# Performance work log

Measured on AMD Instinct MI355X. Metric: run time of the kernel, lower is better.

Reference implementation:

```python
import jax, jax.numpy as jnp
import numpy as np

N, C, V, T = 16, 32, 512, 64
H, EMB, D = 4, 64, 16
OUT_C = 64
BN_EPS = 1e-5


def setup_inputs() -> dict:
    key = jax.random.key(0)
    ks = jax.random.split(key, 12)
    x = jax.random.normal(ks[0], (N, C, V, T), dtype=jnp.float32)
    t_in = jax.random.uniform(ks[1], (N, T), dtype=jnp.float32)
    # random-walk-like supports; scaled so chained nconv hops stay O(1)
    A0 = jax.random.normal(ks[2], (V, V), dtype=jnp.float32) * (V ** -0.5)
    A1 = jax.random.normal(ks[3], (V, V), dtype=jnp.float32) * (V ** -0.5)
    A2 = jax.random.normal(ks[4], (V, V), dtype=jnp.float32) * (V ** -0.5)
    factors = jax.random.normal(ks[5], (H,), dtype=jnp.float32) * 0.1
    Wq = jax.random.normal(ks[6], (H, EMB, D), dtype=jnp.float32) * (EMB ** -0.5)
    Wk = jax.random.normal(ks[7], (H, EMB, D), dtype=jnp.float32) * (EMB ** -0.5)
    GC_IN = 7 * C  # (order*support_len + 1) * in_channels
    W_out = jax.random.normal(ks[8], (OUT_C, GC_IN), dtype=jnp.float32) * (GC_IN ** -0.5)
    b_out = jnp.zeros((OUT_C,), dtype=jnp.float32)
    W_res = jax.random.normal(ks[9], (OUT_C, C), dtype=jnp.float32) * (C ** -0.5)
    b_res = jnp.zeros((OUT_C,), dtype=jnp.float32)
    bn_gamma = jnp.ones((OUT_C,), dtype=jnp.float32)
    bn_beta = jnp.zeros((OUT_C,), dtype=jnp.float32)
    bn_mean = jnp.zeros((OUT_C,), dtype=jnp.float32)
    bn_var = jnp.ones((OUT_C,), dtype=jnp.float32)
    alpha = jnp.full((1,), 0.25, dtype=jnp.float32)  # PReLU init
    return dict(x=x, t_in=t_in, A0=A0, A1=A1, A2=A2, factors=factors,
                Wq=Wq, Wk=Wk, W_out=W_out, b_out=b_out,
                W_res=W_res, b_res=b_res, bn_gamma=bn_gamma, bn_beta=bn_beta,
                bn_mean=bn_mean, bn_var=bn_var, alpha=alpha)


def reference(x, t_in, A0, A1, A2, factors, Wq, Wk, W_out, b_out,
              W_res, b_res, bn_gamma, bn_beta, bn_mean, bn_var, alpha):
    # --- learnEmbedding, all heads at once: emb[b,h,t,f] ---
    div = jnp.arange(0, EMB, 2, dtype=x.dtype)           # [EMB/2]
    div_term = jnp.exp(div[None, :] * factors[:, None])  # [H, EMB/2]
    phase = jnp.einsum('bt,hf->bhtf', t_in, div_term)    # [N,H,T,EMB/2]
    emb = jnp.concatenate([jnp.sin(phase), jnp.cos(phase)], axis=-1)  # [N,H,T,EMB]
    # --- ATT per head (t_out=None => q_emb == k_emb) ---
    q = jnp.einsum('bhtf,hfd->bhtd', emb, Wq)
    k = jnp.einsum('bhtf,hfd->bhtd', emb, Wk)
    att = jax.nn.softmax(jnp.einsum('bhtd,bhpd->bhtp', q, k) / (D ** 0.5), axis=-1)  # [N,H,T,T]
    # --- temporal mixing, summed over heads (matches per-head += loop) ---
    xt = jnp.einsum('ncvt,nhpt->ncvp', x, att)           # [N,C,V,T]
    # --- gcn: diffusion over 3 supports, order 2 ---
    outs = [xt]
    for A in (A0, A1, A2):
        x1 = jnp.einsum('ncvl,vw->ncwl', xt, A)
        x2 = jnp.einsum('ncvl,vw->ncwl', x1, A)
        outs.extend([x1, x2])
    h = jnp.concatenate(outs, axis=1)                    # [N,7C,V,T]
    # --- 1x1 output projection ---
    y = jnp.einsum('ncvt,oc->novt', h, W_out) + b_out[None, :, None, None]
    # --- residual branch: 1x1 conv + BatchNorm (eval) ---
    r = jnp.einsum('ncvt,oc->novt', x, W_res) + b_res[None, :, None, None]
    r = (r - bn_mean[None, :, None, None]) * jax.lax.rsqrt(bn_var + BN_EPS)[None, :, None, None]
    r = r * bn_gamma[None, :, None, None] + bn_beta[None, :, None, None]
    # --- residual add + PReLU (dropout is identity in eval) ---
    out = y + r
    out = jnp.where(out > 0, out, alpha[0] * out)
    return out
```

## Files before the change

### kernel.cpp

```cpp
#include <hip/hip_runtime.h>

namespace {
constexpr int N_ = 16, C_ = 32, V_ = 512, T_ = 64;
constexpr int H_ = 4, D_ = 16, OC_ = 64;
constexpr int EMB_ = 64;
constexpr int GCIN_ = 7 * C_;
constexpr int TV_ = T_ * V_;
}

typedef _Float16 f16x8 __attribute__((ext_vector_type(8)));
typedef _Float16 f16x4 __attribute__((ext_vector_type(4)));
typedef float f32x4 __attribute__((ext_vector_type(4)));

__global__ __launch_bounds__(64) void att_kernel(
    const float* __restrict__ t_in, const float* __restrict__ factors,
    const float* __restrict__ Wq, const float* __restrict__ Wk,
    float* __restrict__ att)
{
    const int n = blockIdx.x >> 2;
    const int h = blockIdx.x & 3;
    const int t = threadIdx.x;

    __shared__ float wq_l[EMB_][D_];
    __shared__ float wk_l[EMB_][D_];
    __shared__ float k_l[T_][D_ + 1];

#pragma unroll
    for (int d = 0; d < D_; ++d) {
        wq_l[t][d] = Wq[(h * EMB_ + t) * D_ + d];
        wk_l[t][d] = Wk[(h * EMB_ + t) * D_ + d];
    }
    __syncthreads();

    const float tv = t_in[n * T_ + t];
    const float fh = factors[h];
    float emb[EMB_];
#pragma unroll
    for (int j = 0; j < 32; ++j) {
        float dt = __expf((float)(2 * j) * fh);
        float ph = tv * dt;
        float s, c;
        __sincosf(ph, &s, &c);
        emb[j] = s;
        emb[j + 32] = c;
    }

    float q[D_];
#pragma unroll
    for (int d = 0; d < D_; ++d) {
        float aq = 0.f, ak = 0.f;
#pragma unroll
        for (int f = 0; f < EMB_; ++f) {
            aq += emb[f] * wq_l[f][d];
            ak += emb[f] * wk_l[f][d];
        }
        q[d] = aq;
        k_l[t][d] = ak;
    }
    __syncthreads();

    float L[T_];
    float m = -1e30f;
#pragma unroll
    for (int j = 0; j < T_; ++j) {
        float a = 0.f;
#pragma unroll
        for (int d = 0; d < D_; ++d) a += q[d] * k_l[j][d];
        a *= 0.25f;
        L[j] = a;
        m = fmaxf(m, a);
    }
    float ssum = 0.f;
#pragma unroll
    for (int j = 0; j < T_; ++j) {
        float e = __expf(L[j] - m);
        L[j] = e;
        ssum += e;
    }
    const float inv = 1.f / ssum;
    float* arow = att + (((size_t)(n * H_ + h) * T_ + t) * T_);
#pragma unroll
    for (int j = 0; j < T_; ++j) arow[j] = L[j] * inv;
}

__global__ __launch_bounds__(256) void sred_kernel(
    const float* __restrict__ att, float* __restrict__ S)
{
    int g = blockIdx.x * 256 + threadIdx.x;
    if (g >= N_ * T_ * T_) return;
    int n = g / (T_ * T_);
    int ij = g - n * (T_ * T_);
    float a = 0.f;
#pragma unroll
    for (int h = 0; h < H_; ++h) a += att[(size_t)(n * H_ + h) * (T_ * T_) + ij];
    S[g] = a;
}

__global__ __launch_bounds__(256) void prepAt_kernel(
    const float* __restrict__ A0, const float* __restrict__ A1,
    const float* __restrict__ A2, _Float16* __restrict__ At16)
{
    const int s = blockIdx.z;
    const float* A = (s == 0) ? A0 : ((s == 1) ? A1 : A2);
    const int v0 = blockIdx.y * 32, w0 = blockIdx.x * 32;
    const int tid = threadIdx.x;
    __shared__ float sT[32][33];
#pragma unroll
    for (int k = 0; k < 4; ++k) {
        int lin = k * 256 + tid;
        int i = lin >> 5, w = lin & 31;
        sT[i][w] = A[(size_t)(v0 + i) * V_ + w0 + w];
    }
    __syncthreads();
#pragma unroll
    for (int k = 0; k < 4; ++k) {
        int lin = k * 256 + tid;
        int j = lin >> 5, i = lin & 31;
        At16[(size_t)s * V_ * V_ + (size_t)(w0 + j) * V_ + v0 + i] = (_Float16)sT[i][j];
    }
}

__global__ __launch_bounds__(256) void prepxT_kernel(
    const float* __restrict__ x, _Float16* __restrict__ xT, int n0)
{
    const int b = blockIdx.z;
    const int v0 = blockIdx.x * 32;
    const int t0 = blockIdx.y * 32;
    const int tid = threadIdx.x;
    __shared__ float sT[32][33];
    const float* xb = x + ((size_t)(n0 * C_) + b) * (size_t)(V_ * T_);
    {
        int vi = tid >> 3, tq = tid & 7;
        *(float4*)&sT[vi][tq * 4] = *(const float4*)&xb[(size_t)(v0 + vi) * T_ + t0 + tq * 4];
    }
    __syncthreads();
    {
        int tj = tid >> 3, vq = tid & 7;
        f16x4 o4;
        o4[0] = (_Float16)sT[vq * 4 + 0][tj];
        o4[1] = (_Float16)sT[vq * 4 + 1][tj];
        o4[2] = (_Float16)sT[vq * 4 + 2][tj];
        o4[3] = (_Float16)sT[vq * 4 + 3][tj];
        *(f16x4*)&xT[(size_t)b * TV_ + (size_t)(t0 + tj) * V_ + v0 + vq * 4] = o4;
    }
}

__global__ __launch_bounds__(256) void prepW_kernel(
    const float* __restrict__ W_out, const float* __restrict__ b_out,
    const float* __restrict__ W_res, const float* __restrict__ b_res,
    const float* __restrict__ gamma, const float* __restrict__ beta,
    const float* __restrict__ mean, const float* __restrict__ var,
    _Float16* __restrict__ Wcat, float* __restrict__ bias)
{
    const int tid = threadIdx.x;
    const int o = tid & 63;
    const int kb = tid >> 6;
    const float rs = gamma[o] * rsqrtf(var[o] + 1e-5f);
    for (int kk = 0; kk < 64; ++kk) {
        int k = kb * 64 + kk;
        float w = (k < GCIN_) ? W_out[o * GCIN_ + k] : rs * W_res[o * C_ + (k - GCIN_)];
        Wcat[o * 256 + k] = (_Float16)w;
    }
    if (tid < 64) bias[tid] = b_out[tid] + beta[tid] + rs * (b_res[tid] - mean[tid]);
}

__global__ __launch_bounds__(256) void xtT_kernel(
    const float* __restrict__ x, const float* __restrict__ S,
    _Float16* __restrict__ XT, int n0)
{
    const int b = blockIdx.y;
    const int n = n0 + b / C_;
    const int lane = threadIdx.x & 63;
    const int wav = threadIdx.x >> 6;
    const int vbase = blockIdx.x * 256 + wav * 64;
    const int row16 = lane & 15;
    const int kg = lane >> 4;

    const float* Sn = S + (size_t)n * (T_ * T_);
    const float* xb = x + ((size_t)(n0 * C_) + b) * (V_ * T_);

    f32x4 acc[4][4];
#pragma unroll
    for (int i = 0; i < 4; ++i)
#pragma unroll
        for (int j = 0; j < 4; ++j) acc[i][j] = (f32x4){0.f, 0.f, 0.f, 0.f};

#pragma unroll
    for (int ks = 0; ks < 2; ++ks) {
        f16x8 a[4], bf[4];
#pragma unroll
        for (int mt = 0; mt < 4; ++mt) {
            const float* p = xb + (size_t)(vbase + mt * 16 + row16) * T_ + ks * 32 + kg * 8;
            float4 u = *(const float4*)p;
            float4 w = *(const float4*)(p + 4);
            f16x8 t8;
            t8[0] = (_Float16)u.x; t8[1] = (_Float16)u.y; t8[2] = (_Float16)u.z; t8[3] = (_Float16)u.w;
            t8[4] = (_Float16)w.x; t8[5] = (_Float16)w.y; t8[6] = (_Float16)w.z; t8[7] = (_Float16)w.w;
            a[mt] = t8;
        }
#pragma unroll
        for (int nt = 0; nt < 4; ++nt) {
            const float* p = Sn + (size_t)(nt * 16 + row16) * T_ + ks * 32 + kg * 8;
            float4 u = *(const float4*)p;
            float4 w = *(const float4*)(p + 4);
            f16x8 t8;
            t8[0] = (_Float16)u.x; t8[1] = (_Float16)u.y; t8[2] = (_Float16)u.z; t8[3] = (_Float16)u.w;
            t8[4] = (_Float16)w.x; t8[5] = (_Float16)w.y; t8[6] = (_Float16)w.z; t8[7] = (_Float16)w.w;
            bf[nt] = t8;
        }
#pragma unroll
        for (int nt = 0; nt < 4; ++nt)
#pragma unroll
            for (int mt = 0; mt < 4; ++mt)
                acc[mt][nt] = __builtin_amdgcn_mfma_f32_16x16x32_f16(a[mt], bf[nt], acc[mt][nt], 0, 0, 0);
    }

    _Float16* Yb = XT + (size_t)b * TV_;
#pragma unroll
    for (int mt = 0; mt < 4; ++mt)
#pragma unroll
        for (int nt = 0; nt < 4; ++nt) {
            int p = nt * 16 + row16;
            int v = vbase + mt * 16 + kg * 4;
            f16x4 h;
            h[0] = (_Float16)acc[mt][nt][0];
            h[1] = (_Float16)acc[mt][nt][1];
            h[2] = (_Float16)acc[mt][nt][2];
            h[3] = (_Float16)acc[mt][nt][3];
            *(f16x4*)&Yb[(size_t)p * V_ + v] = h;
        }
}

__global__ __launch_bounds__(512) void hopf_kernel(
    const _Float16* __restrict__ At16, _Float16* __restrict__ Hb,
    unsigned long long ASZ)
{
    const int bp = blockIdx.x;
    const int s = blockIdx.y;
    const int tid = threadIdx.x;
    const int lane = tid & 63;
    const int wav = tid >> 6;
    const int wbase = wav * 64;
    const int row16 = lane & 15;
    const int kg = lane >> 4;

    __shared__ _Float16 xs0[T_ * V_];
    __shared__ _Float16 xs1[T_ * V_];

    const _Float16* At = At16 + (size_t)s * V_ * V_;
    const int b0 = bp * 2;
    const _Float16* Xb0 = Hb + (size_t)b0 * TV_;
    const _Float16* Xb1 = Hb + (size_t)(b0 + 1) * TV_;
    _Float16* Y1a = Hb + (size_t)(1 + 2 * s) * ASZ + (size_t)b0 * TV_;
    _Float16* Y1b = Y1a + TV_;
    _Float16* Y2a = Hb + (size_t)(2 + 2 * s) * ASZ + (size_t)b0 * TV_;
    _Float16* Y2b = Y2a + TV_;

    const _Float16* ax = At + (size_t)(wbase + row16) * V_ + kg * 8;

    f32x4 acc0[4][4], acc1[4][4];
    f16x8 aC[4], aN[4];

#pragma unroll
    for (int k = 0; k < 8; ++k) {
        int lin = k * 512 + tid;
        int t = lin >> 6;
        int v8 = (lin & 63) << 3;
        int byte = (t * V_ + v8) * 2;
        f16x8 v0v = *(const f16x8*)&Xb0[(size_t)t * V_ + v8];
        f16x8 v1v = *(const f16x8*)&Xb1[(size_t)t * V_ + v8];
        *(f16x8*)((char*)xs0 + (byte ^ ((t & 7) << 4))) = v0v;
        *(f16x8*)((char*)xs1 + (byte ^ ((t & 7) << 4))) = v1v;
    }
    __syncthreads();

#pragma unroll
    for (int i = 0; i < 4; ++i)
#pragma unroll
        for (int j = 0; j < 4; ++j) {
            acc0[i][j] = (f32x4){0.f, 0.f, 0.f, 0.f};
            acc1[i][j] = (f32x4){0.f, 0.f, 0.f, 0.f};
        }
#pragma unroll
    for (int i = 0; i < 4; ++i)
        aC[i] = *(const f16x8*)(ax + (size_t)i * 16 * V_);

#pragma unroll
    for (int it = 0; it < 16; ++it) {
        const int v0 = it * 32;
        if (it < 15) {
#pragma unroll
            for (int i = 0; i < 4; ++i)
                aN[i] = *(const f16x8*)(ax + (size_t)i * 16 * V_ + v0 + 32);
        }
        f16x8 b0v[4], b1v[4];
#pragma unroll
        for (int nt = 0; nt < 4; ++nt) {
            int t = nt * 16 + row16;
            int byte = (t * V_ + v0 + kg * 8) * 2;
            b0v[nt] = *(const f16x8*)((const char*)xs0 + (byte ^ ((t & 7) << 4)));
            b1v[nt] = *(const f16x8*)((const char*)xs1 + (byte ^ ((t & 7) << 4)));
        }
        __builtin_amdgcn_s_setprio(1);
#pragma unroll
        for (int nt = 0; nt < 4; ++nt)
#pragma unroll
            for (int mt = 0; mt < 4; ++mt) {
                acc0[mt][nt] = __builtin_amdgcn_mfma_f32_16x16x32_f16(aC[mt], b0v[nt], acc0[mt][nt], 0, 0, 0);
                acc1[mt][nt] = __builtin_amdgcn_mfma_f32_16x16x32_f16(aC[mt], b1v[nt], acc1[mt][nt], 0, 0, 0);
            }
        __builtin_amdgcn_s_setprio(0);
#pragma unroll
        for (int i = 0; i < 4; ++i) aC[i] = aN[i];
    }
    __syncthreads();

#pragma unroll
    for (int mt = 0; mt < 4; ++mt)
#pragma unroll
        for (int nt = 0; nt < 4; ++nt) {
            int t = nt * 16 + row16;
            int w = wbase + mt * 16 + kg * 4;
            int byte = (t * V_ + w) * 2;
            f16x4 h0, h1;
            h0[0] = (_Float16)acc0[mt][nt][0]; h0[1] = (_Float16)acc0[mt][nt][1];
            h0[2] = (_Float16)acc0[mt][nt][2]; h0[3] = (_Float16)acc0[mt][nt][3];
            h1[0] = (_Float16)acc1[mt][nt][0]; h1[1] = (_Float16)acc1[mt][nt][1];
            h1[2] = (_Float16)acc1[mt][nt][2]; h1[3] = (_Float16)acc1[mt][nt][3];
            *(f16x4*)((char*)xs0 + (byte ^ ((t & 7) << 4))) = h0;
            *(f16x4*)((char*)xs1 + (byte ^ ((t & 7) << 4))) = h1;
        }
    __syncthreads();

#pragma unroll
    for (int mt = 0; mt < 4; ++mt)
#pragma unroll
        for (int nt = 0; nt < 4; ++nt) {
            int t = nt * 16 + row16;
            int w = wbase + mt * 16 + kg * 4;
            f16x4 h0;
            h0[0] = (_Float16)acc0[mt][nt][0]; h0[1] = (_Float16)acc0[mt][nt][1];
            h0[2] = (_Float16)acc0[mt][nt][2]; h0[3] = (_Float16)acc0[mt][nt][3];
            *(f16x4*)&Y1a[(size_t)t * V_ + w] = h0;
        }
#pragma unroll
    for (int mt = 0; mt < 4; ++mt)
#pragma unroll
        for (int nt = 0; nt < 4; ++nt) {
            int t = nt * 16 + row16;
            int w = wbase + mt * 16 + kg * 4;
            f16x4 h1;
            h1[0] = (_Float16)acc1[mt][nt][0]; h1[1] = (_Float16)acc1[mt][nt][1];
            h1[2] = (_Float16)acc1[mt][nt][2]; h1[3] = (_Float16)acc1[mt][nt][3];
            *(f16x4*)&Y1b[(size_t)t * V_ + w] = h1;
        }

#pragma unroll
    for (int i = 0; i < 4; ++i)
#pragma unroll
        for (int j = 0; j < 4; ++j) {
            acc0[i][j] = (f32x4){0.f, 0.f, 0.f, 0.f};
            acc1[i][j] = (f32x4){0.f, 0.f, 0.f, 0.f};
        }
#pragma unroll
    for (int i = 0; i < 4; ++i)
        aC[i] = *(const f16x8*)(ax + (size_t)i * 16 * V_);

#pragma unroll
    for (int it = 0; it < 16; ++it) {
        const int v0 = it * 32;
        if (it < 15) {
#pragma unroll
            for (int i = 0; i < 4; ++i)
                aN[i] = *(const f16x8*)(ax + (size_t)i * 16 * V_ + v0 + 32);
        }
        f16x8 b0v[4], b1v[4];
#pragma unroll
        for (int nt = 0; nt < 4; ++nt) {
            int t = nt * 16 + row16;
            int byte = (t * V_ + v0 + kg * 8) * 2;
            b0v[nt] = *(const f16x8*)((const char*)xs0 + (byte ^ ((t & 7) << 4)));
            b1v[nt] = *(const f16x8*)((const char*)xs1 + (byte ^ ((t & 7) << 4)));
        }
        __builtin_amdgcn_s_setprio(1);
#pragma unroll
        for (int nt = 0; nt < 4; ++nt)
#pragma unroll
            for (int mt = 0; mt < 4; ++mt) {
                acc0[mt][nt] = __builtin_amdgcn_mfma_f32_16x16x32_f16(aC[mt], b0v[nt], acc0[mt][nt], 0, 0, 0);
                acc1[mt][nt] = __builtin_amdgcn_mfma_f32_16x16x32_f16(aC[mt], b1v[nt], acc1[mt][nt], 0, 0, 0);
            }
        __builtin_amdgcn_s_setprio(0);
#pragma unroll
        for (int i = 0; i < 4; ++i) aC[i] = aN[i];
    }

#pragma unroll
    for (int mt = 0; mt < 4; ++mt)
#pragma unroll
        for (int nt = 0; nt < 4; ++nt) {
            int t = nt * 16 + row16;
            int w = wbase + mt * 16 + kg * 4;
            f16x4 h0;
            h0[0] = (_Float16)acc0[mt][nt][0]; h0[1] = (_Float16)acc0[mt][nt][1];
            h0[2] = (_Float16)acc0[mt][nt][2]; h0[3] = (_Float16)acc0[mt][nt][3];
            *(f16x4*)&Y2a[(size_t)t * V_ + w] = h0;
        }
#pragma unroll
    for (int mt = 0; mt < 4; ++mt)
#pragma unroll
        for (int nt = 0; nt < 4; ++nt) {
            int t = nt * 16 + row16;
            int w = wbase + mt * 16 + kg * 4;
            f16x4 h1;
            h1[0] = (_Float16)acc1[mt][nt][0]; h1[1] = (_Float16)acc1[mt][nt][1];
            h1[2] = (_Float16)acc1[mt][nt][2]; h1[3] = (_Float16)acc1[mt][nt][3];
            *(f16x4*)&Y2b[(size_t)t * V_ + w] = h1;
        }
}

__global__ __launch_bounds__(256) void epi_kernel(
    const _Float16* __restrict__ H, unsigned long long ASZ,
    const _Float16* __restrict__ Wcat, const float* __restrict__ bias,
    const float* __restrict__ alpha_p, float* __restrict__ out, int n0)
{
    const int v0 = blockIdx.x * 32;
    const int t0 = blockIdx.y * 8;
    const int nl = blockIdx.z;
    const int ng = n0 + nl;
    const int tid = threadIdx.x;
    const int lane = tid & 63;
    const int wv = tid >> 6;
    const int row16 = lane & 15;
    const int kg = lane >> 4;

    f32x4 acc[2][2][4];
#pragma unroll
    for (int j = 0; j < 2; ++j)
#pragma unroll
        for (int vs = 0; vs < 2; ++vs)
#pragma unroll
            for (int mt = 0; mt < 4; ++mt) acc[j][vs][mt] = (f32x4){0.f, 0.f, 0.f, 0.f};

    const size_t pb = ((size_t)(nl * C_ + kg * 8)) * TV_
                    + (size_t)(t0 + wv * 2) * V_ + v0 + row16;

#pragma unroll
    for (int ks = 0; ks < 8; ++ks) {
        const _Float16* Hk = H + (size_t)ks * ASZ;
        f16x8 a[4];
#pragma unroll
        for (int mt = 0; mt < 4; ++mt)
            a[mt] = *(const f16x8*)(Wcat + (mt * 16 + row16) * 256 + ks * 32 + kg * 8);
#pragma unroll
        for (int j = 0; j < 2; ++j)
#pragma unroll
            for (int vs = 0; vs < 2; ++vs) {
                const _Float16* hp = Hk + pb + (size_t)j * V_ + vs * 16;
                f16x8 bf;
#pragma unroll
                for (int e = 0; e < 8; ++e) bf[e] = hp[(size_t)e * TV_];
#pragma unroll
                for (int mt = 0; mt < 4; ++mt)
                    acc[j][vs][mt] = __builtin_amdgcn_mfma_f32_16x16x32_f16(a[mt], bf, acc[j][vs][mt], 0, 0, 0);
            }
    }

    __shared__ float sC[16 * 33 * 9];
    const float al = alpha_p[0];
    const int ot = tid >> 4;
    const int vvt = tid & 15;

    for (int mt = 0; mt < 4; ++mt) {
#pragma unroll
        for (int j = 0; j < 2; ++j)
#pragma unroll
            for (int vs = 0; vs < 2; ++vs)
#pragma unroll
                for (int r = 0; r < 4; ++r)
                    sC[((kg * 4 + r) * 33 + vs * 16 + row16) * 9 + wv * 2 + j] = acc[j][vs][mt][r];
        __syncthreads();
        const float bo = bias[mt * 16 + ot];
#pragma unroll
        for (int vh = 0; vh < 2; ++vh) {
            const int vl = vvt + vh * 16;
            float vals[8];
#pragma unroll
            for (int tt = 0; tt < 8; ++tt) {
                float u = sC[(ot * 33 + vl) * 9 + tt] + bo;
                vals[tt] = u > 0.f ? u : al * u;
            }
            float* op = out + (((size_t)ng * OC_ + mt * 16 + ot) * V_ + v0 + vl) * T_ + t0;
            *(float4*)&op[0] = make_float4(vals[0], vals[1], vals[2], vals[3]);
            *(float4*)&op[4] = make_float4(vals[4], vals[5], vals[6], vals[7]);
        }
        __syncthreads();
    }
}

extern "C" void kernel_launch(void* const* d_in, const int* in_sizes, int n_in,
                              void* d_out, int out_size, void* d_ws, size_t ws_size,
                              hipStream_t stream)
{
    const float* x       = (const float*)d_in[0];
    const float* t_in    = (const float*)d_in[1];
    const float* A0      = (const float*)d_in[2];
    const float* A1      = (const float*)d_in[3];
    const float* A2      = (const float*)d_in[4];
    const float* factors = (const float*)d_in[5];
    const float* Wq      = (const float*)d_in[6];
    const float* Wk      = (const float*)d_in[7];
    const float* W_out   = (const float*)d_in[8];
    const float* b_out   = (const float*)d_in[9];
    const float* W_res   = (const float*)d_in[10];
    const float* b_res   = (const float*)d_in[11];
    const float* gamma   = (const float*)d_in[12];
    const float* beta    = (const float*)d_in[13];
    const float* mean    = (const float*)d_in[14];
    const float* var     = (const float*)d_in[15];
    const float* alpha   = (const float*)d_in[16];
    float* out = (float*)d_out;

    float* att = (float*)d_ws;
    float* S    = att + (size_t)N_ * H_ * T_ * T_;
    float* bias = S + (size_t)N_ * T_ * T_;
    _Float16* At16 = (_Float16*)(bias + 64);
    _Float16* Wcat = At16 + (size_t)3 * V_ * V_;
    _Float16* Hbase = Wcat + (size_t)64 * 256;

    const size_t fixed = ((size_t)N_ * H_ * T_ * T_ + (size_t)N_ * T_ * T_ + 64) * 4
                       + ((size_t)3 * V_ * V_ + 64 * 256) * 2;
    int Nc = 16;
    while (Nc > 1 && fixed + (size_t)8 * Nc * C_ * T_ * V_ * 2 > ws_size) Nc >>= 1;
    const size_t ASZ = (size_t)Nc * C_ * T_ * V_;

    att_kernel<<<N_ * H_, 64, 0, stream>>>(t_in, factors, Wq, Wk, att);
    sred_kernel<<<(N_ * T_ * T_ + 255) / 256, 256, 0, stream>>>(att, S);
    prepAt_kernel<<<dim3(16, 16, 3), 256, 0, stream>>>(A0, A1, A2, At16);
    prepW_kernel<<<1, 256, 0, stream>>>(W_out, b_out, W_res, b_res,
                                        gamma, beta, mean, var, Wcat, bias);

    for (int n0 = 0; n0 < N_; n0 += Nc) {
        const int nsl = Nc * C_;
        xtT_kernel<<<dim3(2, nsl), 256, 0, stream>>>(x, S, Hbase, n0);
        prepxT_kernel<<<dim3(16, 2, nsl), 256, 0, stream>>>(x, Hbase + (size_t)7 * ASZ, n0);
        hopf_kernel<<<dim3(nsl / 2, 3), 512, 0, stream>>>(At16, Hbase, (unsigned long long)ASZ);
        epi_kernel<<<dim3(16, 8, Nc), 256, 0, stream>>>(
            Hbase, (unsigned long long)ASZ, Wcat, bias, alpha, out, n0);
    }
}
```

Measured before the change: 495.1 us.

## Interleave channel pairs in fp16 intermediate buffers for wider epilogue loads

Changes the fp16 intermediate layout so each pair of channels is interleaved element-wise. The producers (xtT, prepxT, hopf) now process two channels per block and write 16-byte vectors, hopf de-interleaves into LDS, and the epilogue reads channel pairs as 2-element loads instead of 8 scalar strided loads. This is meant to cut scattered narrow global loads in the epilogue and halve the store instruction count. It also removes the s_setprio hints around the MFMA blocks in hopf and adds shuffle work when filling LDS.

```diff
diff --git a/kernel.cpp b/kernel.cpp
--- a/kernel.cpp
+++ b/kernel.cpp
@@ -10,6 +10,7 @@
 
 typedef _Float16 f16x8 __attribute__((ext_vector_type(8)));
 typedef _Float16 f16x4 __attribute__((ext_vector_type(4)));
+typedef _Float16 f16x2 __attribute__((ext_vector_type(2)));
 typedef float f32x4 __attribute__((ext_vector_type(4)));
 
 __global__ __launch_bounds__(64) void att_kernel(
@@ -123,25 +124,29 @@
 __global__ __launch_bounds__(256) void prepxT_kernel(
     const float* __restrict__ x, _Float16* __restrict__ xT, int n0)
 {
-    const int b = blockIdx.z;
+    const int q = blockIdx.z;
     const int v0 = blockIdx.x * 32;
     const int t0 = blockIdx.y * 32;
     const int tid = threadIdx.x;
-    __shared__ float sT[32][33];
-    const float* xb = x + ((size_t)(n0 * C_) + b) * (size_t)(V_ * T_);
+    __shared__ float sT0[32][33];
+    __shared__ float sT1[32][33];
+    const float* xb0 = x + ((size_t)(n0 * C_) + 2 * q) * (size_t)(V_ * T_);
+    const float* xb1 = xb0 + (size_t)(V_ * T_);
     {
         int vi = tid >> 3, tq = tid & 7;
-        *(float4*)&sT[vi][tq * 4] = *(const float4*)&xb[(size_t)(v0 + vi) * T_ + t0 + tq * 4];
+        *(float4*)&sT0[vi][tq * 4] = *(const float4*)&xb0[(size_t)(v0 + vi) * T_ + t0 + tq * 4];
+        *(float4*)&sT1[vi][tq * 4] = *(const float4*)&xb1[(size_t)(v0 + vi) * T_ + t0 + tq * 4];
     }
     __syncthreads();
     {
         int tj = tid >> 3, vq = tid & 7;
-        f16x4 o4;
-        o4[0] = (_Float16)sT[vq * 4 + 0][tj];
-        o4[1] = (_Float16)sT[vq * 4 + 1][tj];
-        o4[2] = (_Float16)sT[vq * 4 + 2][tj];
-        o4[3] = (_Float16)sT[vq * 4 + 3][tj];
-        *(f16x4*)&xT[(size_t)b * TV_ + (size_t)(t0 + tj) * V_ + v0 + vq * 4] = o4;
+        f16x8 o;
+#pragma unroll
+        for (int j = 0; j < 4; ++j) {
+            o[2 * j]     = (_Float16)sT0[vq * 4 + j][tj];
+            o[2 * j + 1] = (_Float16)sT1[vq * 4 + j][tj];
+        }
+        *(f16x8*)&xT[(size_t)q * 2 * TV_ + ((size_t)(t0 + tj) * V_ + v0 + vq * 4) * 2] = o;
     }
 }
 
@@ -168,41 +173,47 @@
     const float* __restrict__ x, const float* __restrict__ S,
     _Float16* __restrict__ XT, int n0)
 {
-    const int b = blockIdx.y;
-    const int n = n0 + b / C_;
+    const int q = blockIdx.y;
+    const int n = q >> 4;
     const int lane = threadIdx.x & 63;
     const int wav = threadIdx.x >> 6;
     const int vbase = blockIdx.x * 256 + wav * 64;
     const int row16 = lane & 15;
     const int kg = lane >> 4;
 
-    const float* Sn = S + (size_t)n * (T_ * T_);
-    const float* xb = x + ((size_t)(n0 * C_) + b) * (V_ * T_);
-
-    f32x4 acc[4][4];
+    const float* Sn = S + (size_t)(n0 + n) * (T_ * T_);
+    const float* xb0 = x + ((size_t)(n0 * C_) + 2 * q) * (size_t)(V_ * T_);
+    const float* xb1 = xb0 + (size_t)(V_ * T_);
+
+    f32x4 acc0[4][4], acc1[4][4];
 #pragma unroll
     for (int i = 0; i < 4; ++i)
 #pragma unroll
-        for (int j = 0; j < 4; ++j) acc[i][j] = (f32x4){0.f, 0.f, 0.f, 0.f};
+        for (int j = 0; j < 4; ++j) {
+            acc0[i][j] = (f32x4){0.f, 0.f, 0.f, 0.f};
+            acc1[i][j] = (f32x4){0.f, 0.f, 0.f, 0.f};
+        }
 
 #pragma unroll
     for (int ks = 0; ks < 2; ++ks) {
-        f16x8 a[4], bf[4];
+        f16x8 a0[4], a1[4], bf[4];
 #pragma unroll
         for (int mt = 0; mt < 4; ++mt) {
-            const float* p = xb + (size_t)(vbase + mt * 16 + row16) * T_ + ks * 32 + kg * 8;
-            float4 u = *(const float4*)p;
-            float4 w = *(const float4*)(p + 4);
-            f16x8 t8;
-            t8[0] = (_Float16)u.x; t8[1] = (_Float16)u.y; t8[2] = (_Float16)u.z; t8[3] = (_Float16)u.w;
-            t8[4] = (_Float16)w.x; t8[5] = (_Float16)w.y; t8[6] = (_Float16)w.z; t8[7] = (_Float16)w.w;
-            a[mt] = t8;
+            const float* p0 = xb0 + (size_t)(vbase + mt * 16 + row16) * T_ + ks * 32 + kg * 8;
+            const float* p1 = xb1 + (size_t)(vbase + mt * 16 + row16) * T_ + ks * 32 + kg * 8;
+            float4 u0 = *(const float4*)p0, w0 = *(const float4*)(p0 + 4);
+            float4 u1 = *(const float4*)p1, w1 = *(const float4*)(p1 + 4);
+            f16x8 t0, t1;
+            t0[0] = (_Float16)u0.x; t0[1] = (_Float16)u0.y; t0[2] = (_Float16)u0.z; t0[3] = (_Float16)u0.w;
+            t0[4] = (_Float16)w0.x; t0[5] = (_Float16)w0.y; t0[6] = (_Float16)w0.z; t0[7] = (_Float16)w0.w;
+            t1[0] = (_Float16)u1.x; t1[1] = (_Float16)u1.y; t1[2] = (_Float16)u1.z; t1[3] = (_Float16)u1.w;
+            t1[4] = (_Float16)w1.x; t1[5] = (_Float16)w1.y; t1[6] = (_Float16)w1.z; t1[7] = (_Float16)w1.w;
+            a0[mt] = t0; a1[mt] = t1;
         }
 #pragma unroll
         for (int nt = 0; nt < 4; ++nt) {
             const float* p = Sn + (size_t)(nt * 16 + row16) * T_ + ks * 32 + kg * 8;
-            float4 u = *(const float4*)p;
-            float4 w = *(const float4*)(p + 4);
+            float4 u = *(const float4*)p, w = *(const float4*)(p + 4);
             f16x8 t8;
             t8[0] = (_Float16)u.x; t8[1] = (_Float16)u.y; t8[2] = (_Float16)u.z; t8[3] = (_Float16)u.w;
             t8[4] = (_Float16)w.x; t8[5] = (_Float16)w.y; t8[6] = (_Float16)w.z; t8[7] = (_Float16)w.w;
@@ -211,23 +222,26 @@
 #pragma unroll
         for (int nt = 0; nt < 4; ++nt)
 #pragma unroll
-            for (int mt = 0; mt < 4; ++mt)
-                acc[mt][nt] = __builtin_amdgcn_mfma_f32_16x16x32_f16(a[mt], bf[nt], acc[mt][nt], 0, 0, 0);
-    }
-
-    _Float16* Yb = XT + (size_t)b * TV_;
+            for (int mt = 0; mt < 4; ++mt) {
+                acc0[mt][nt] = __builtin_amdgcn_mfma_f32_16x16x32_f16(a0[mt], bf[nt], acc0[mt][nt], 0, 0, 0);
+                acc1[mt][nt] = __builtin_amdgcn_mfma_f32_16x16x32_f16(a1[mt], bf[nt], acc1[mt][nt], 0, 0, 0);
+            }
+    }
+
+    _Float16* Yq = XT + (size_t)q * 2 * TV_;
 #pragma unroll
     for (int mt = 0; mt < 4; ++mt)
 #pragma unroll
         for (int nt = 0; nt < 4; ++nt) {
             int p = nt * 16 + row16;
             int v = vbase + mt * 16 + kg * 4;
-            f16x4 h;
-            h[0] = (_Float16)acc[mt][nt][0];
-            h[1] = (_Float16)acc[mt][nt][1];
-            h[2] = (_Float16)acc[mt][nt][2];
-            h[3] = (_Float16)acc[mt][nt][3];
-            *(f16x4*)&Yb[(size_t)p * V_ + v] = h;
+            f16x8 h;
+#pragma unroll
+            for (int r = 0; r < 4; ++r) {
+                h[2 * r]     = (_Float16)acc0[mt][nt][r];
+                h[2 * r + 1] = (_Float16)acc1[mt][nt][r];
+            }
+            *(f16x8*)&Yq[((size_t)p * V_ + v) * 2] = h;
         }
 }
 
@@ -248,13 +262,9 @@
     __shared__ _Float16 xs1[T_ * V_];
 
     const _Float16* At = At16 + (size_t)s * V_ * V_;
-    const int b0 = bp * 2;
-    const _Float16* Xb0 = Hb + (size_t)b0 * TV_;
-    const _Float16* Xb1 = Hb + (size_t)(b0 + 1) * TV_;
-    _Float16* Y1a = Hb + (size_t)(1 + 2 * s) * ASZ + (size_t)b0 * TV_;
-    _Float16* Y1b = Y1a + TV_;
-    _Float16* Y2a = Hb + (size_t)(2 + 2 * s) * ASZ + (size_t)b0 * TV_;
-    _Float16* Y2b = Y2a + TV_;
+    const _Float16* Xi = Hb + (size_t)bp * 2 * TV_;
+    _Float16* Y1i = Hb + (size_t)(1 + 2 * s) * ASZ + (size_t)bp * 2 * TV_;
+    _Float16* Y2i = Hb + (size_t)(2 + 2 * s) * ASZ + (size_t)bp * 2 * TV_;
 
     const _Float16* ax = At + (size_t)(wbase + row16) * V_ + kg * 8;
 
@@ -266,11 +276,16 @@
         int lin = k * 512 + tid;
         int t = lin >> 6;
         int v8 = (lin & 63) << 3;
+        const f16x8 lo = *(const f16x8*)&Xi[((size_t)t * V_ + v8) * 2];
+        const f16x8 hi = *(const f16x8*)&Xi[((size_t)t * V_ + v8) * 2 + 8];
+        f16x8 s0, s1;
+        s0[0] = lo[0]; s0[1] = lo[2]; s0[2] = lo[4]; s0[3] = lo[6];
+        s0[4] = hi[0]; s0[5] = hi[2]; s0[6] = hi[4]; s0[7] = hi[6];
+        s1[0] = lo[1]; s1[1] = lo[3]; s1[2] = lo[5]; s1[3] = lo[7];
+        s1[4] = hi[1]; s1[5] = hi[3]; s1[6] = hi[5]; s1[7] = hi[7];
         int byte = (t * V_ + v8) * 2;
-        f16x8 v0v = *(const f16x8*)&Xb0[(size_t)t * V_ + v8];
-        f16x8 v1v = *(const f16x8*)&Xb1[(size_t)t * V_ + v8];
-        *(f16x8*)((char*)xs0 + (byte ^ ((t & 7) << 4))) = v0v;
-        *(f16x8*)((char*)xs1 + (byte ^ ((t & 7) << 4))) = v1v;
+        *(f16x8*)((char*)xs0 + (byte ^ ((t & 7) << 4))) = s0;
+        *(f16x8*)((char*)xs1 + (byte ^ ((t & 7) << 4))) = s1;
     }
     __syncthreads();
 
@@ -301,7 +316,6 @@
             b0v[nt] = *(const f16x8*)((const char*)xs0 + (byte ^ ((t & 7) << 4)));
             b1v[nt] = *(const f16x8*)((const char*)xs1 + (byte ^ ((t & 7) << 4)));
         }
-        __builtin_amdgcn_s_setprio(1);
 #pragma unroll
         for (int nt = 0; nt < 4; ++nt)
 #pragma unroll
@@ -309,7 +323,6 @@
                 acc0[mt][nt] = __builtin_amdgcn_mfma_f32_16x16x32_f16(aC[mt], b0v[nt], acc0[mt][nt], 0, 0, 0);
                 acc1[mt][nt] = __builtin_amdgcn_mfma_f32_16x16x32_f16(aC[mt], b1v[nt], acc1[mt][nt], 0, 0, 0);
             }
-        __builtin_amdgcn_s_setprio(0);
 #pragma unroll
         for (int i = 0; i < 4; ++i) aC[i] = aN[i];
     }
@@ -338,21 +351,13 @@
         for (int nt = 0; nt < 4; ++nt) {
             int t = nt * 16 + row16;
             int w = wbase + mt * 16 + kg * 4;
-            f16x4 h0;
-            h0[0] = (_Float16)acc0[mt][nt][0]; h0[1] = (_Float16)acc0[mt][nt][1];
-            h0[2] = (_Float16)acc0[mt][nt][2]; h0[3] = (_Float16)acc0[mt][nt][3];
-            *(f16x4*)&Y1a[(size_t)t * V_ + w] = h0;
-        }
-#pragma unroll
-    for (int mt = 0; mt < 4; ++mt)
-#pragma unroll
-        for (int nt = 0; nt < 4; ++nt) {
-            int t = nt * 16 + row16;
-            int w = wbase + mt * 16 + kg * 4;
-            f16x4 h1;
-            h1[0] = (_Float16)acc1[mt][nt][0]; h1[1] = (_Float16)acc1[mt][nt][1];
-            h1[2] = (_Float16)acc1[mt][nt][2]; h1[3] = (_Float16)acc1[mt][nt][3];
-            *(f16x4*)&Y1b[(size_t)t * V_ + w] = h1;
+            f16x8 h;
+#pragma unroll
+            for (int r = 0; r < 4; ++r) {
+                h[2 * r]     = (_Float16)acc0[mt][nt][r];
+                h[2 * r + 1] = (_Float16)acc1[mt][nt][r];
+            }
+            *(f16x8*)&Y1i[((size_t)t * V_ + w) * 2] = h;
         }
 
 #pragma unroll
@@ -382,7 +387,6 @@
             b0v[nt] = *(const f16x8*)((const char*)xs0 + (byte ^ ((t & 7) << 4)));
             b1v[nt] = *(const f16x8*)((const char*)xs1 + (byte ^ ((t & 7) << 4)));
         }
-        __builtin_amdgcn_s_setprio(1);
 #pragma unroll
         for (int nt = 0; nt < 4; ++nt)
 #pragma unroll
@@ -390,7 +394,6 @@
                 acc0[mt][nt] = __builtin_amdgcn_mfma_f32_16x16x32_f16(aC[mt], b0v[nt], acc0[mt][nt], 0, 0, 0);
                 acc1[mt][nt] = __builtin_amdgcn_mfma_f32_16x16x32_f16(aC[mt], b1v[nt], acc1[mt][nt], 0, 0, 0);
             }
-        __builtin_amdgcn_s_setprio(0);
 #pragma unroll
         for (int i = 0; i < 4; ++i) aC[i] = aN[i];
     }
@@ -401,21 +404,13 @@
         for (int nt = 0; nt < 4; ++nt) {
             int t = nt * 16 + row16;
             int w = wbase + mt * 16 + kg * 4;
-            f16x4 h0;
-            h0[0] = (_Float16)acc0[mt][nt][0]; h0[1] = (_Float16)acc0[mt][nt][1];
-            h0[2] = (_Float16)acc0[mt][nt][2]; h0[3] = (_Float16)acc0[mt][nt][3];
-            *(f16x4*)&Y2a[(size_t)t * V_ + w] = h0;
-        }
-#pragma unroll
-    for (int mt = 0; mt < 4; ++mt)
-#pragma unroll
-        for (int nt = 0; nt < 4; ++nt) {
-            int t = nt * 16 + row16;
-            int w = wbase + mt * 16 + kg * 4;
-            f16x4 h1;
-            h1[0] = (_Float16)acc1[mt][nt][0]; h1[1] = (_Float16)acc1[mt][nt][1];
-            h1[2] = (_Float16)acc1[mt][nt][2]; h1[3] = (_Float16)acc1[mt][nt][3];
-            *(f16x4*)&Y2b[(size_t)t * V_ + w] = h1;
+            f16x8 h;
+#pragma unroll
+            for (int r = 0; r < 4; ++r) {
+                h[2 * r]     = (_Float16)acc0[mt][nt][r];
+                h[2 * r + 1] = (_Float16)acc1[mt][nt][r];
+            }
+            *(f16x8*)&Y2i[((size_t)t * V_ + w) * 2] = h;
         }
 }
 
@@ -442,8 +437,8 @@
 #pragma unroll
             for (int mt = 0; mt < 4; ++mt) acc[j][vs][mt] = (f32x4){0.f, 0.f, 0.f, 0.f};
 
-    const size_t pb = ((size_t)(nl * C_ + kg * 8)) * TV_
-                    + (size_t)(t0 + wv * 2) * V_ + v0 + row16;
+    const size_t pbI = ((size_t)(nl * 16 + kg * 4)) * 2 * TV_
+                     + ((size_t)(t0 + wv * 2) * V_ + v0 + row16) * 2;
 
 #pragma unroll
     for (int ks = 0; ks < 8; ++ks) {
@@ -456,10 +451,14 @@
         for (int j = 0; j < 2; ++j)
 #pragma unroll
             for (int vs = 0; vs < 2; ++vs) {
-                const _Float16* hp = Hk + pb + (size_t)j * V_ + vs * 16;
+                const _Float16* hp = Hk + pbI + ((size_t)j * V_ + vs * 16) * 2;
                 f16x8 bf;
 #pragma unroll
-                for (int e = 0; e < 8; ++e) bf[e] = hp[(size_t)e * TV_];
+                for (int qq = 0; qq < 4; ++qq) {
+                    f16x2 pr = *(const f16x2*)(hp + (size_t)qq * 2 * TV_);
+                    bf[2 * qq]     = pr[0];
+                    bf[2 * qq + 1] = pr[1];
+                }
 #pragma unroll
                 for (int mt = 0; mt < 4; ++mt)
                     acc[j][vs][mt] = __builtin_amdgcn_mfma_f32_16x16x32_f16(a[mt], bf, acc[j][vs][mt], 0, 0, 0);
@@ -542,8 +541,8 @@
 
     for (int n0 = 0; n0 < N_; n0 += Nc) {
         const int nsl = Nc * C_;
-        xtT_kernel<<<dim3(2, nsl), 256, 0, stream>>>(x, S, Hbase, n0);
-        prepxT_kernel<<<dim3(16, 2, nsl), 256, 0, stream>>>(x, Hbase + (size_t)7 * ASZ, n0);
+        xtT_kernel<<<dim3(2, nsl / 2), 256, 0, stream>>>(x, S, Hbase, n0);
+        prepxT_kernel<<<dim3(16, 2, nsl / 2), 256, 0, stream>>>(x, Hbase + (size_t)7 * ASZ, n0);
         hopf_kernel<<<dim3(nsl / 2, 3), 512, 0, stream>>>(At16, Hbase, (unsigned long long)ASZ);
         epi_kernel<<<dim3(16, 8, Nc), 256, 0, stream>>>(
             Hbase, (unsigned long long)ASZ, Wcat, bias, alpha, out, n0);
```

New measurement: 453.4 us (median of 3 runs). 8.4% less time.
